# Kernel optimization log

Measured on AMD Instinct MI355X. Metric: run time of the kernel, lower is better.

## Reference

```python
import jax, jax.numpy as jnp
import numpy as np

N_SPOT, N_CITY, N_WORD = 20000, 2000, 20000
E_HAS, E_IN, E_DESC, E_RDESC = 100000, 100000, 400000, 400000
HID = 256


def setup_inputs() -> dict:
    key = jax.random.key(0)
    ks = jax.random.split(key, 48)

    def g(i, shape, s):
        return jax.random.normal(ks[i], shape, dtype=jnp.float32) * s

    inp = {}
    inp['x_spot'] = g(0, (N_SPOT, 2560), 0.5)
    inp['x_city'] = g(1, (N_CITY, 128), 0.5)
    inp['x_word'] = g(2, (N_WORD, 300), 0.5)
    inp['W_att'] = g(3, (4, 512, 128), 0.05)  # 4 heads, per_dim=128
    inp['q_att'] = g(4, (4, 128), 0.1)
    i = 5
    for n, d in [('w1_has_s', 128), ('w1_has_t', 512), ('w1_in_s', 512), ('w1_in_t', 128),
                 ('w1_desc_s', 300), ('w1_desc_t', 512), ('w1_rdesc_s', 512), ('w1_rdesc_t', 300)]:
        inp[n] = g(i, (d, HID), 0.05); i += 1
    for n in ['w2_has_s', 'w2_has_t', 'w2_in_s', 'w2_in_t', 'w2_desc_s', 'w2_desc_t', 'w2_rdesc_s', 'w2_rdesc_t']:
        inp[n] = g(i, (HID, HID), 0.05); i += 1
    for n in ['wl_spot', 'wl_city', 'wl_word']:
        inp[n] = g(i, (HID, 1), 0.05); i += 1
    for n in ['bl_spot', 'bl_city', 'bl_word']:
        inp[n] = jnp.zeros((1,), jnp.float32)
    for n, e, hi in [('e_has_src', E_HAS, N_CITY), ('e_has_tgt', E_HAS, N_SPOT),
                     ('e_in_src', E_IN, N_SPOT), ('e_in_tgt', E_IN, N_CITY),
                     ('e_desc_src', E_DESC, N_WORD), ('e_desc_tgt', E_DESC, N_SPOT),
                     ('e_rdesc_src', E_RDESC, N_SPOT), ('e_rdesc_tgt', E_RDESC, N_WORD)]:
        inp[n] = jax.random.randint(ks[i], (e,), 0, hi, dtype=jnp.int32); i += 1
    return inp


def _attention(x, W_att, q_att):
    # AttentionModule(input_dim=512, num_heads=4, split=5): (N, 2560) -> (N, 512)
    x = x.reshape(-1, 5, 512)
    xw = jnp.einsum('nsi,hio->hnso', x, W_att)                      # (4,N,5,128)
    a = jax.nn.leaky_relu(jnp.einsum('hnso,ho->hns', xw, q_att), 0.2)
    a = jax.nn.softmax(a, axis=2)                                   # softmax over split dim
    out = jnp.einsum('hnso,hns->hno', xw, a)                        # (4,N,128)
    return jnp.transpose(out, (1, 0, 2)).reshape(x.shape[0], 4 * 128)


def _scatter_mean(src, idx, n):
    s = jax.ops.segment_sum(src, idx, num_segments=n)
    c = jax.ops.segment_sum(jnp.ones((src.shape[0], 1), src.dtype), idx, num_segments=n)
    return s / jnp.maximum(c, 1.0)


def _edge(x_s, x_t, w_s, w_t, src, tgt):
    # per-edge-type linear, gather on source index, scatter-mean into targets
    msg = (x_s @ w_s)[src]
    return x_t @ w_t + _scatter_mean(msg, tgt, x_t.shape[0])


def _conv(xs, xc, xw, w, e):
    spot = _edge(xc, xs, w['has_s'], w['has_t'], e['has_src'], e['has_tgt']) \
         + _edge(xw, xs, w['desc_s'], w['desc_t'], e['desc_src'], e['desc_tgt'])
    city = _edge(xs, xc, w['in_s'], w['in_t'], e['in_src'], e['in_tgt'])
    word = _edge(xs, xw, w['rdesc_s'], w['rdesc_t'], e['rdesc_src'], e['rdesc_tgt'])
    # div[spot]=2, div[city]=div[word]=1; ReLU flag applies a second (idempotent) relu
    return jax.nn.relu(spot * 0.5), jax.nn.relu(city), jax.nn.relu(word)


def reference(x_spot, x_city, x_word, W_att, q_att,
              w1_has_s, w1_has_t, w1_in_s, w1_in_t, w1_desc_s, w1_desc_t, w1_rdesc_s, w1_rdesc_t,
              w2_has_s, w2_has_t, w2_in_s, w2_in_t, w2_desc_s, w2_desc_t, w2_rdesc_s, w2_rdesc_t,
              wl_spot, bl_spot, wl_city, bl_city, wl_word, bl_word,
              e_has_src, e_has_tgt, e_in_src, e_in_tgt, e_desc_src, e_desc_tgt, e_rdesc_src, e_rdesc_tgt):
    e = dict(has_src=e_has_src, has_tgt=e_has_tgt, in_src=e_in_src, in_tgt=e_in_tgt,
             desc_src=e_desc_src, desc_tgt=e_desc_tgt, rdesc_src=e_rdesc_src, rdesc_tgt=e_rdesc_tgt)
    w1 = dict(has_s=w1_has_s, has_t=w1_has_t, in_s=w1_in_s, in_t=w1_in_t,
              desc_s=w1_desc_s, desc_t=w1_desc_t, rdesc_s=w1_rdesc_s, rdesc_t=w1_rdesc_t)
    w2 = dict(has_s=w2_has_s, has_t=w2_has_t, in_s=w2_in_s, in_t=w2_in_t,
              desc_s=w2_desc_s, desc_t=w2_desc_t, rdesc_s=w2_rdesc_s, rdesc_t=w2_rdesc_t)
    xs = _attention(x_spot, W_att, q_att)  # multi=True path
    s1, c1, wd1 = _conv(xs, x_city, x_word, w1, e)
    s2, c2, wd2 = _conv(s1, c1, wd1, w2, e)
    out_spot = s2 @ wl_spot + bl_spot
    out_city = c2 @ wl_city + bl_city
    out_word = wd2 @ wl_word + bl_word
    # concat=True: mean over the two layer outputs per node type
    return ((s1 + s2) * 0.5, (c1 + c2) * 0.5, (wd1 + wd2) * 0.5, out_spot, out_city, out_word)
```

## Files before the change

### kernel.cpp

```cpp
#include <hip/hip_runtime.h>
#include <hip/hip_bf16.h>

#define HID 256
#define NSPOT 20000
#define NCITY 2000
#define NWORD 20000

typedef __attribute__((ext_vector_type(8))) short bhalf8;
typedef __attribute__((ext_vector_type(4))) float floatx4;

__global__ void wq_kernel(const float* __restrict__ W, const float* __restrict__ q,
                          float* __restrict__ wq) {
    int idx = blockIdx.x * 256 + threadIdx.x;
    if (idx >= 2048) return;
    int h = idx >> 9, i = idx & 511;
    const float* Wr = W + ((size_t)h * 512 + i) * 128;
    const float* qr = q + h * 128;
    float s = 0.f;
    #pragma unroll 4
    for (int o = 0; o < 128; o++) s += Wr[o] * qr[o];
    wq[idx] = s;
}

__global__ __launch_bounds__(256) void attn_kernel(const float* __restrict__ x,
                                                   const float* __restrict__ wq,
                                                   __hip_bfloat16* __restrict__ xbar) {
    __shared__ float xl[2560];
    __shared__ float al[4][8];
    int n = blockIdx.x;
    int tid = threadIdx.x;
    int wave = tid >> 6, lane = tid & 63;
    const float4* xr4 = (const float4*)(x + (size_t)n * 2560);
    for (int i = tid; i < 640; i += 256) ((float4*)xl)[i] = xr4[i];
    __syncthreads();
    const float* wqh = wq + wave * 512;
    for (int s = 0; s < 5; s++) {
        float a = 0.f;
        #pragma unroll
        for (int j = 0; j < 8; j++)
            a += xl[s * 512 + lane + j * 64] * wqh[lane + j * 64];
        #pragma unroll
        for (int off = 32; off > 0; off >>= 1) a += __shfl_down(a, off, 64);
        if (lane == 0) al[wave][s] = a;
    }
    __syncthreads();
    if (tid < 4) {
        float z[5]; float m = -1e30f;
        #pragma unroll
        for (int s = 0; s < 5; s++) {
            float v = al[tid][s];
            v = (v >= 0.f) ? v : 0.2f * v;
            z[s] = v; m = fmaxf(m, v);
        }
        float e[5]; float sum = 0.f;
        #pragma unroll
        for (int s = 0; s < 5; s++) { e[s] = __expf(z[s] - m); sum += e[s]; }
        float r = 1.f / sum;
        #pragma unroll
        for (int s = 0; s < 5; s++) al[tid][s] = e[s] * r;
    }
    __syncthreads();
    float a0 = al[wave][0], a1 = al[wave][1], a2 = al[wave][2], a3 = al[wave][3], a4 = al[wave][4];
    __hip_bfloat16* xo = xbar + ((size_t)wave * NSPOT + n) * 512;
    #pragma unroll
    for (int j = 0; j < 8; j++) {
        int i = lane + j * 64;
        float v = a0 * xl[i] + a1 * xl[512 + i] + a2 * xl[1024 + i] + a3 * xl[1536 + i] + a4 * xl[2048 + i];
        xo[i] = __float2bfloat16(v);
    }
}

#define KP 40
__global__ __launch_bounds__(256) void gemm_bf16(
    const __hip_bfloat16* __restrict__ A, int lda, long sA,
    const __hip_bfloat16* __restrict__ Bt, int ldb, long sB,
    float* __restrict__ C, int ldc,
    __hip_bfloat16* __restrict__ Cb, int ldcb, long sCb,
    int M, int N, int K) {
    __shared__ short As[128 * KP];
    __shared__ short Bs[128 * KP];
    int z = blockIdx.z;
    A += (size_t)z * sA;
    Bt += (size_t)z * sB;
    if (Cb) Cb += (size_t)z * sCb;
    int tid = threadIdx.x;
    int wave = tid >> 6, lane = tid & 63;
    int wr = wave & 1, wc = wave >> 1;
    int quad = lane >> 4, l16 = lane & 15;
    int rowbase = blockIdx.x * 128;
    int colbase = blockIdx.y * 128;
    int srow = tid >> 2;
    int skoff = (tid & 3) * 8;
    floatx4 acc[4][4];
    #pragma unroll
    for (int i = 0; i < 4; i++)
        #pragma unroll
        for (int j = 0; j < 4; j++)
            acc[i][j] = (floatx4){0.f, 0.f, 0.f, 0.f};

    for (int k0 = 0; k0 < K; k0 += 32) {
        #pragma unroll
        for (int i = 0; i < 2; i++) {
            int r = srow + i * 64;
            int gr = rowbase + r;
            int4 va = make_int4(0, 0, 0, 0);
            if (gr < M) va = *(const int4*)(A + (size_t)gr * lda + k0 + skoff);
            *(int4*)(As + r * KP + skoff) = va;
            int4 vb = *(const int4*)(Bt + (size_t)(colbase + r) * ldb + k0 + skoff);
            *(int4*)(Bs + r * KP + skoff) = vb;
        }
        __syncthreads();
        bhalf8 af[4], bfr[4];
        #pragma unroll
        for (int rt = 0; rt < 4; rt++)
            af[rt] = *(const bhalf8*)(As + (wr * 64 + rt * 16 + l16) * KP + quad * 8);
        #pragma unroll
        for (int ct = 0; ct < 4; ct++)
            bfr[ct] = *(const bhalf8*)(Bs + (wc * 64 + ct * 16 + l16) * KP + quad * 8);
        #pragma unroll
        for (int rt = 0; rt < 4; rt++)
            #pragma unroll
            for (int ct = 0; ct < 4; ct++)
                acc[rt][ct] = __builtin_amdgcn_mfma_f32_16x16x32_bf16(af[rt], bfr[ct], acc[rt][ct], 0, 0, 0);
        __syncthreads();
    }
    #pragma unroll
    for (int rt = 0; rt < 4; rt++) {
        #pragma unroll
        for (int r = 0; r < 4; r++) {
            int grow = rowbase + wr * 64 + rt * 16 + quad * 4 + r;
            if (grow < M) {
                #pragma unroll
                for (int ct = 0; ct < 4; ct++) {
                    int gcol = colbase + wc * 64 + ct * 16 + l16;
                    float v = acc[rt][ct][r];
                    if (C)  C[(size_t)grow * ldc + gcol] = v;
                    if (Cb) Cb[(size_t)grow * ldcb + gcol] = __float2bfloat16(v);
                }
            }
        }
    }
}

struct GemmDesc {
    const __hip_bfloat16* A;
    const __hip_bfloat16* Bt;
    float* C;
    __hip_bfloat16* Cb;
    int lda, ldb, ldc, ldcb, M, K;
};
struct GemmDesc8 { GemmDesc d[8]; };

__global__ __launch_bounds__(256) void gemm_bf16_grouped(GemmDesc8 descs) {
    GemmDesc g = descs.d[blockIdx.z];
    int rowbase = blockIdx.x * 128;
    if (rowbase >= g.M) return;
    __shared__ short As[128 * KP];
    __shared__ short Bs[128 * KP];
    int tid = threadIdx.x;
    int wave = tid >> 6, lane = tid & 63;
    int wr = wave & 1, wc = wave >> 1;
    int quad = lane >> 4, l16 = lane & 15;
    int colbase = blockIdx.y * 128;
    int srow = tid >> 2;
    int skoff = (tid & 3) * 8;
    floatx4 acc[4][4];
    #pragma unroll
    for (int i = 0; i < 4; i++)
        #pragma unroll
        for (int j = 0; j < 4; j++)
            acc[i][j] = (floatx4){0.f, 0.f, 0.f, 0.f};

    for (int k0 = 0; k0 < g.K; k0 += 32) {
        #pragma unroll
        for (int i = 0; i < 2; i++) {
            int r = srow + i * 64;
            int gr = rowbase + r;
            int4 va = make_int4(0, 0, 0, 0);
            if (gr < g.M) va = *(const int4*)(g.A + (size_t)gr * g.lda + k0 + skoff);
            *(int4*)(As + r * KP + skoff) = va;
            int4 vb = *(const int4*)(g.Bt + (size_t)(colbase + r) * g.ldb + k0 + skoff);
            *(int4*)(Bs + r * KP + skoff) = vb;
        }
        __syncthreads();
        bhalf8 af[4], bfr[4];
        #pragma unroll
        for (int rt = 0; rt < 4; rt++)
            af[rt] = *(const bhalf8*)(As + (wr * 64 + rt * 16 + l16) * KP + quad * 8);
        #pragma unroll
        for (int ct = 0; ct < 4; ct++)
            bfr[ct] = *(const bhalf8*)(Bs + (wc * 64 + ct * 16 + l16) * KP + quad * 8);
        #pragma unroll
        for (int rt = 0; rt < 4; rt++)
            #pragma unroll
            for (int ct = 0; ct < 4; ct++)
                acc[rt][ct] = __builtin_amdgcn_mfma_f32_16x16x32_bf16(af[rt], bfr[ct], acc[rt][ct], 0, 0, 0);
        __syncthreads();
    }
    #pragma unroll
    for (int rt = 0; rt < 4; rt++) {
        #pragma unroll
        for (int r = 0; r < 4; r++) {
            int grow = rowbase + wr * 64 + rt * 16 + quad * 4 + r;
            if (grow < g.M) {
                #pragma unroll
                for (int ct = 0; ct < 4; ct++) {
                    int gcol = colbase + wc * 64 + ct * 16 + l16;
                    float v = acc[rt][ct][r];
                    if (g.C)  g.C[(size_t)grow * g.ldc + gcol] = v;
                    if (g.Cb) g.Cb[(size_t)grow * g.ldcb + gcol] = __float2bfloat16(v);
                }
            }
        }
    }
}

struct TDesc { const float* in; __hip_bfloat16* out; int K; int N; int Kp; };
struct TDesc8 { TDesc d[8]; };
__global__ void transpose_cast_kernel(TDesc8 descs) {
    TDesc dsc = descs.d[blockIdx.z];
    __shared__ float tile[32][33];
    int k0 = blockIdx.x * 32, n0 = blockIdx.y * 32;
    if (k0 >= dsc.Kp || n0 >= dsc.N) return;
    int tn = threadIdx.x & 31, t8 = threadIdx.x >> 5;
    #pragma unroll
    for (int i = 0; i < 4; i++) {
        int k = k0 + t8 * 4 + i;
        float v = 0.f;
        if (k < dsc.K && n0 + tn < dsc.N) v = dsc.in[(size_t)k * dsc.N + n0 + tn];
        tile[t8 * 4 + i][tn] = v;
    }
    __syncthreads();
    int kk = threadIdx.x & 31, n8 = threadIdx.x >> 5;
    #pragma unroll
    for (int i = 0; i < 4; i++) {
        int n = n0 + n8 * 4 + i;
        int k = k0 + kk;
        if (n < dsc.N && k < dsc.Kp)
            dsc.out[(size_t)n * dsc.Kp + k] = __float2bfloat16(tile[kk][n8 * 4 + i]);
    }
}

__global__ void cast_kernel(const float* __restrict__ in, __hip_bfloat16* __restrict__ out, int n) {
    int i = blockIdx.x * 256 + threadIdx.x;
    if (i < n) out[i] = __float2bfloat16(in[i]);
}

__global__ void cast_pad_kernel(const float* __restrict__ in, __hip_bfloat16* __restrict__ out,
                                int rows, int K, int Kp) {
    int idx = blockIdx.x * 256 + threadIdx.x;
    if (idx >= rows * Kp) return;
    int r = idx / Kp, k = idx - r * Kp;
    out[idx] = (k < K) ? __float2bfloat16(in[(size_t)r * K + k]) : __float2bfloat16(0.f);
}

struct EdgeDesc { const int* src; const int* tgt; int E; int n;
                  int* deg; int* rp; int* cur; int* cs; };
struct EdgeDesc4 { EdgeDesc d[4]; };

__global__ void hist4_kernel(EdgeDesc4 ds) {
    EdgeDesc d = ds.d[blockIdx.y];
    int e = blockIdx.x * 256 + threadIdx.x;
    if (e < d.E) atomicAdd(&d.deg[d.tgt[e]], 1);
}

__global__ void scan4_kernel(EdgeDesc4 ds) {
    EdgeDesc dd = ds.d[blockIdx.x];
    __shared__ int partx[257];
    __shared__ int part[256];
    int tid = threadIdx.x;
    int n = dd.n;
    int chunk = (n + 255) / 256;
    int lo = tid * chunk;
    int hi = lo + chunk; if (hi > n) hi = n;
    int s = 0;
    for (int i = lo; i < hi; i++) s += dd.deg[i];
    part[tid] = s;
    __syncthreads();
    if (tid == 0) {
        int acc = 0;
        for (int i = 0; i < 256; i++) { partx[i] = acc; acc += part[i]; }
        partx[256] = acc;
    }
    __syncthreads();
    int acc = partx[tid];
    for (int i = lo; i < hi; i++) { dd.rp[i] = acc; dd.cur[i] = acc; acc += dd.deg[i]; }
    if (tid == 0) dd.rp[n] = partx[256];
}

__global__ void fill4_kernel(EdgeDesc4 ds) {
    EdgeDesc d = ds.d[blockIdx.y];
    int e = blockIdx.x * 256 + threadIdx.x;
    if (e >= d.E) return;
    int t = d.tgt[e];
    int pos = atomicAdd(&d.cur[t], 1);
    d.cs[pos] = d.src[e];
}

struct AggDesc { const __hip_bfloat16* msg; const int* rp; const int* cs; float* outm; };
struct AggDesc4 { AggDesc d[4]; int start1, start2, start3; };

__global__ __launch_bounds__(256) void agg4_kernel(AggDesc4 ds) {
    int bid = blockIdx.x;
    int gi = (bid >= ds.start1) + (bid >= ds.start2) + (bid >= ds.start3);
    int base = (gi == 0) ? 0 : (gi == 1) ? ds.start1 : (gi == 2) ? ds.start2 : ds.start3;
    AggDesc g = ds.d[gi];
    int t = bid - base;
    int d = threadIdx.x;
    int lo = g.rp[t], hi = g.rp[t + 1];
    float acc = 0.f;
    int i = lo;
    for (; i + 4 <= hi; i += 4) {
        int s0 = g.cs[i], s1 = g.cs[i + 1], s2 = g.cs[i + 2], s3 = g.cs[i + 3];
        float m0 = __bfloat162float(g.msg[(size_t)s0 * HID + d]);
        float m1 = __bfloat162float(g.msg[(size_t)s1 * HID + d]);
        float m2 = __bfloat162float(g.msg[(size_t)s2 * HID + d]);
        float m3 = __bfloat162float(g.msg[(size_t)s3 * HID + d]);
        acc += m0 + m1 + m2 + m3;
    }
    for (; i < hi; i++) acc += __bfloat162float(g.msg[(size_t)g.cs[i] * HID + d]);
    g.outm[(size_t)t * HID + d] = acc / fmaxf((float)(hi - lo), 1.f);
}

__global__ void combine_all(const float* Sa, const float* Sb, const float* mH, const float* mD,
                            float* so, __hip_bfloat16* sob,
                            const float* Sc, const float* mI, float* co, __hip_bfloat16* cob,
                            const float* Sw, const float* mR, float* wo, __hip_bfloat16* wob) {
    int bid = blockIdx.x;
    int tid = threadIdx.x;
    if (bid < NSPOT) {
        int idx = bid * 256 + tid;
        float v = fmaxf((Sa[idx] + Sb[idx] + mH[idx] + mD[idx]) * 0.5f, 0.f);
        so[idx] = v;
        if (sob) sob[idx] = __float2bfloat16(v);
    } else if (bid < NSPOT + NCITY) {
        int idx = (bid - NSPOT) * 256 + tid;
        float v = fmaxf(Sc[idx] + mI[idx], 0.f);
        co[idx] = v;
        if (cob) cob[idx] = __float2bfloat16(v);
    } else {
        int idx = (bid - NSPOT - NCITY) * 256 + tid;
        float v = fmaxf(Sw[idx] + mR[idx], 0.f);
        wo[idx] = v;
        if (wob) wob[idx] = __float2bfloat16(v);
    }
}

__global__ void mean3_kernel(const float* a0, const float* b0, float* o0, int n0,
                             const float* a1, const float* b1, float* o1, int n1,
                             const float* a2, const float* b2, float* o2, int n2) {
    int i = blockIdx.x * 256 + threadIdx.x;
    const float* a; const float* b; float* o;
    if (i < n0) { a = a0; b = b0; o = o0; }
    else if (i < n0 + n1) { a = a1; b = b1; o = o1; i -= n0; }
    else if (i < n0 + n1 + n2) { a = a2; b = b2; o = o2; i -= n0 + n1; }
    else return;
    float4 x = reinterpret_cast<const float4*>(a)[i];
    float4 y = reinterpret_cast<const float4*>(b)[i];
    reinterpret_cast<float4*>(o)[i] =
        make_float4((x.x + y.x) * 0.5f, (x.y + y.y) * 0.5f, (x.z + y.z) * 0.5f, (x.w + y.w) * 0.5f);
}

__global__ void rowdot3_kernel(const float* X0, const float* w0, const float* b0, float* o0, int B0,
                               const float* X1, const float* w1, const float* b1, float* o1, int B1,
                               const float* X2, const float* w2, const float* b2, float* o2, int B2) {
    int bid = blockIdx.x;
    const float* X; const float* w; const float* b; float* o; int M;
    if (bid < B0) { X = X0; w = w0; b = b0; o = o0; M = B0 * 4; }
    else if (bid < B0 + B1) { X = X1; w = w1; b = b1; o = o1; M = B1 * 4; bid -= B0; }
    else { X = X2; w = w2; b = b2; o = o2; M = B2 * 4; bid -= B0 + B1; }
    int row = bid * 4 + (threadIdx.x >> 6);
    if (row >= M) return;
    int lane = threadIdx.x & 63;
    const float* x = X + (size_t)row * HID;
    float s = 0.f;
    #pragma unroll
    for (int j = 0; j < 4; j++) s += x[lane + j * 64] * w[lane + j * 64];
    #pragma unroll
    for (int off = 32; off > 0; off >>= 1) s += __shfl_down(s, off, 64);
    if (lane == 0) o[row] = s + b[0];
}

extern "C" void kernel_launch(void* const* d_in, const int* in_sizes, int n_in,
                              void* d_out, int out_size, void* d_ws, size_t ws_size,
                              hipStream_t stream) {
    const float* x_spot   = (const float*)d_in[0];
    const float* x_city   = (const float*)d_in[1];
    const float* x_word   = (const float*)d_in[2];
    const float* W_att    = (const float*)d_in[3];
    const float* q_att    = (const float*)d_in[4];
    const float* w1[8] = { (const float*)d_in[5], (const float*)d_in[6], (const float*)d_in[7],
                           (const float*)d_in[8], (const float*)d_in[9], (const float*)d_in[10],
                           (const float*)d_in[11], (const float*)d_in[12] };
    const float* w2[8] = { (const float*)d_in[13], (const float*)d_in[14], (const float*)d_in[15],
                           (const float*)d_in[16], (const float*)d_in[17], (const float*)d_in[18],
                           (const float*)d_in[19], (const float*)d_in[20] };
    const float* wl_spot = (const float*)d_in[21];
    const float* wl_city = (const float*)d_in[22];
    const float* wl_word = (const float*)d_in[23];
    const float* bl_spot = (const float*)d_in[24];
    const float* bl_city = (const float*)d_in[25];
    const float* bl_word = (const float*)d_in[26];
    const int* e_has_src   = (const int*)d_in[27];
    const int* e_has_tgt   = (const int*)d_in[28];
    const int* e_in_src    = (const int*)d_in[29];
    const int* e_in_tgt    = (const int*)d_in[30];
    const int* e_desc_src  = (const int*)d_in[31];
    const int* e_desc_tgt  = (const int*)d_in[32];
    const int* e_rdesc_src = (const int*)d_in[33];
    const int* e_rdesc_tgt = (const int*)d_in[34];
    const int E_has   = in_sizes[27];
    const int E_in    = in_sizes[29];
    const int E_desc  = in_sizes[31];
    const int E_rdesc = in_sizes[33];

    float* out = (float*)d_out;
    float* wsf = (float*)d_ws;
    typedef __hip_bfloat16 bf;

    size_t o = 0;
    auto alloc = [&](size_t nfloats) { float* p = wsf + o; o += (nfloats + 15) & ~(size_t)15; return p; };
    float* wqb       = alloc(2048);
    bf* xs_bf        = (bf*)alloc((size_t)NSPOT * 512 / 2);
    bf* x_city_bf    = (bf*)alloc((size_t)NCITY * 128 / 2);
    bf* x_word_bf    = (bf*)alloc((size_t)NWORD * 320 / 2);
    bf* Wt_att       = (bf*)alloc((size_t)4 * 128 * 512 / 2);
    int K1[8]  = {128, 512, 512, 128, 300, 512, 512, 300};
    int Kp1[8] = {128, 512, 512, 128, 320, 512, 512, 320};
    bf* Wt1[8];
    for (int i = 0; i < 8; i++) Wt1[i] = (bf*)alloc((size_t)256 * Kp1[i] / 2);
    bf* Wt2[8];
    for (int i = 0; i < 8; i++) Wt2[i] = (bf*)alloc((size_t)256 * 256 / 2);
    float* Sa = alloc((size_t)NSPOT * HID);
    float* Sb = alloc((size_t)NSPOT * HID);
    float* Sc = alloc((size_t)NCITY * HID);
    float* Sw = alloc((size_t)NWORD * HID);
    float* m_has   = alloc((size_t)NSPOT * HID);
    float* m_desc  = alloc((size_t)NSPOT * HID);
    float* m_in    = alloc((size_t)NCITY * HID);
    float* m_rdesc = alloc((size_t)NWORD * HID);
    float* s1  = alloc((size_t)NSPOT * HID);
    float* c1  = alloc((size_t)NCITY * HID);
    float* wd1 = alloc((size_t)NWORD * HID);
    size_t regX = o;
    bf* xbar_bf = (bf*)(wsf + regX);
    size_t ox = regX;
    auto allocX = [&](size_t nfloats) { float* p = wsf + ox; ox += (nfloats + 15) & ~(size_t)15; return p; };
    bf* P_has_bf   = (bf*)allocX((size_t)NCITY * HID / 2);
    bf* P_in_bf    = (bf*)allocX((size_t)NSPOT * HID / 2);
    bf* P_desc_bf  = (bf*)allocX((size_t)NWORD * HID / 2);
    bf* P_rdesc_bf = (bf*)allocX((size_t)NSPOT * HID / 2);
    bf* s1b = (bf*)allocX((size_t)NSPOT * HID / 2);
    bf* c1b = (bf*)allocX((size_t)NCITY * HID / 2);
    bf* wd1b = (bf*)allocX((size_t)NWORD * HID / 2);
    o = regX + (size_t)4 * NSPOT * 512 / 2;
    float* s2  = m_has;
    float* c2  = m_in;
    float* wd2 = m_rdesc;
    int* wsi = (int*)(wsf + o);
    size_t io = 0;
    int* deg_has    = wsi + io; io += NSPOT;
    int* deg_desc   = wsi + io; io += NSPOT;
    int* deg_in     = wsi + io; io += NCITY;
    int* deg_rdesc  = wsi + io; io += NWORD;
    size_t deg_bytes = io * sizeof(int);
    int* rp_has     = wsi + io; io += NSPOT + 1;
    int* rp_desc    = wsi + io; io += NSPOT + 1;
    int* rp_in      = wsi + io; io += NCITY + 1;
    int* rp_rdesc   = wsi + io; io += NWORD + 1;
    int* cur_has    = wsi + io; io += NSPOT + 1;
    int* cur_desc   = wsi + io; io += NSPOT + 1;
    int* cur_in     = wsi + io; io += NCITY + 1;
    int* cur_rdesc  = wsi + io; io += NWORD + 1;
    int* cs_has     = wsi + io; io += E_has;
    int* cs_desc    = wsi + io; io += E_desc;
    int* cs_in      = wsi + io; io += E_in;
    int* cs_rdesc   = wsi + io; io += E_rdesc;
    (void)ws_size; (void)n_in; (void)out_size;

    {
        TDesc8 t{};
        for (int i = 0; i < 4; i++)
            t.d[i] = TDesc{ W_att + (size_t)i * 512 * 128, Wt_att + (size_t)i * 128 * 512, 512, 128, 512 };
        hipLaunchKernelGGL(transpose_cast_kernel, dim3(16, 4, 4), dim3(256), 0, stream, t);
    }
    {
        TDesc8 t{};
        for (int i = 0; i < 8; i++) t.d[i] = TDesc{ w1[i], Wt1[i], K1[i], 256, Kp1[i] };
        hipLaunchKernelGGL(transpose_cast_kernel, dim3(16, 8, 8), dim3(256), 0, stream, t);
    }
    {
        TDesc8 t{};
        for (int i = 0; i < 8; i++) t.d[i] = TDesc{ w2[i], Wt2[i], 256, 256, 256 };
        hipLaunchKernelGGL(transpose_cast_kernel, dim3(8, 8, 8), dim3(256), 0, stream, t);
    }
    hipLaunchKernelGGL(cast_kernel, dim3((NCITY * 128 + 255) / 256), dim3(256), 0, stream,
                       x_city, x_city_bf, NCITY * 128);
    hipLaunchKernelGGL(cast_pad_kernel, dim3((NWORD * 320 + 255) / 256), dim3(256), 0, stream,
                       x_word, x_word_bf, NWORD, 300, 320);

    EdgeDesc4 ed;
    ed.d[0] = EdgeDesc{ e_has_src,   e_has_tgt,   E_has,   NSPOT, deg_has,   rp_has,   cur_has,   cs_has };
    ed.d[1] = EdgeDesc{ e_desc_src,  e_desc_tgt,  E_desc,  NSPOT, deg_desc,  rp_desc,  cur_desc,  cs_desc };
    ed.d[2] = EdgeDesc{ e_in_src,    e_in_tgt,    E_in,    NCITY, deg_in,    rp_in,    cur_in,    cs_in };
    ed.d[3] = EdgeDesc{ e_rdesc_src, e_rdesc_tgt, E_rdesc, NWORD, deg_rdesc, rp_rdesc, cur_rdesc, cs_rdesc };
    int Emax = E_has;
    if (E_desc > Emax) Emax = E_desc;
    if (E_in > Emax) Emax = E_in;
    if (E_rdesc > Emax) Emax = E_rdesc;
    hipMemsetAsync((void*)deg_has, 0, deg_bytes, stream);
    hipLaunchKernelGGL(hist4_kernel, dim3((Emax + 255) / 256, 4), dim3(256), 0, stream, ed);
    hipLaunchKernelGGL(scan4_kernel, dim3(4), dim3(256), 0, stream, ed);
    hipLaunchKernelGGL(fill4_kernel, dim3((Emax + 255) / 256, 4), dim3(256), 0, stream, ed);

    hipLaunchKernelGGL(wq_kernel, dim3(8), dim3(256), 0, stream, W_att, q_att, wqb);
    hipLaunchKernelGGL(attn_kernel, dim3(NSPOT), dim3(256), 0, stream, x_spot, wqb, xbar_bf);
    {
        dim3 g((NSPOT + 127) / 128, 1, 4);
        hipLaunchKernelGGL(gemm_bf16, g, dim3(256), 0, stream,
                           xbar_bf, 512, (long)NSPOT * 512, Wt_att, 512, (long)128 * 512,
                           nullptr, 0, xs_bf, 512, 128, NSPOT, 128, 512);
    }

    int gx = (NSPOT + 127) / 128;

    {
        GemmDesc8 gd;
        gd.d[0] = GemmDesc{ x_city_bf, Wt1[0], nullptr, P_has_bf,   128, 128, 0, HID, NCITY, 128 };
        gd.d[1] = GemmDesc{ xs_bf,     Wt1[1], Sa,      nullptr,    512, 512, HID, 0, NSPOT, 512 };
        gd.d[2] = GemmDesc{ xs_bf,     Wt1[2], nullptr, P_in_bf,    512, 512, 0, HID, NSPOT, 512 };
        gd.d[3] = GemmDesc{ x_city_bf, Wt1[3], Sc,      nullptr,    128, 128, HID, 0, NCITY, 128 };
        gd.d[4] = GemmDesc{ x_word_bf, Wt1[4], nullptr, P_desc_bf,  320, 320, 0, HID, NWORD, 320 };
        gd.d[5] = GemmDesc{ xs_bf,     Wt1[5], Sb,      nullptr,    512, 512, HID, 0, NSPOT, 512 };
        gd.d[6] = GemmDesc{ xs_bf,     Wt1[6], nullptr, P_rdesc_bf, 512, 512, 0, HID, NSPOT, 512 };
        gd.d[7] = GemmDesc{ x_word_bf, Wt1[7], Sw,      nullptr,    320, 320, HID, 0, NWORD, 320 };
        hipLaunchKernelGGL(gemm_bf16_grouped, dim3(gx, 2, 8), dim3(256), 0, stream, gd);
    }

    AggDesc4 ag;
    ag.start1 = NSPOT; ag.start2 = 2 * NSPOT; ag.start3 = 2 * NSPOT + NCITY;
    int agg_blocks = 2 * NSPOT + NCITY + NWORD;
    ag.d[0] = AggDesc{ P_has_bf,   rp_has,   cs_has,   m_has };
    ag.d[1] = AggDesc{ P_desc_bf,  rp_desc,  cs_desc,  m_desc };
    ag.d[2] = AggDesc{ P_in_bf,    rp_in,    cs_in,    m_in };
    ag.d[3] = AggDesc{ P_rdesc_bf, rp_rdesc, cs_rdesc, m_rdesc };
    hipLaunchKernelGGL(agg4_kernel, dim3(agg_blocks), dim3(256), 0, stream, ag);
    hipLaunchKernelGGL(combine_all, dim3(NSPOT + NCITY + NWORD), dim3(256), 0, stream,
                       Sa, Sb, m_has, m_desc, s1, s1b,
                       Sc, m_in, c1, c1b,
                       Sw, m_rdesc, wd1, wd1b);

    {
        GemmDesc8 gd;
        gd.d[0] = GemmDesc{ c1b,  Wt2[0], nullptr, P_has_bf,   HID, HID, 0, HID, NCITY, HID };
        gd.d[1] = GemmDesc{ s1b,  Wt2[1], Sa,      nullptr,    HID, HID, HID, 0, NSPOT, HID };
        gd.d[2] = GemmDesc{ s1b,  Wt2[2], nullptr, P_in_bf,    HID, HID, 0, HID, NSPOT, HID };
        gd.d[3] = GemmDesc{ c1b,  Wt2[3], Sc,      nullptr,    HID, HID, HID, 0, NCITY, HID };
        gd.d[4] = GemmDesc{ wd1b, Wt2[4], nullptr, P_desc_bf,  HID, HID, 0, HID, NWORD, HID };
        gd.d[5] = GemmDesc{ s1b,  Wt2[5], Sb,      nullptr,    HID, HID, HID, 0, NSPOT, HID };
        gd.d[6] = GemmDesc{ s1b,  Wt2[6], nullptr, P_rdesc_bf, HID, HID, 0, HID, NSPOT, HID };
        gd.d[7] = GemmDesc{ wd1b, Wt2[7], Sw,      nullptr,    HID, HID, HID, 0, NWORD, HID };
        hipLaunchKernelGGL(gemm_bf16_grouped, dim3(gx, 2, 8), dim3(256), 0, stream, gd);
    }

    hipLaunchKernelGGL(agg4_kernel, dim3(agg_blocks), dim3(256), 0, stream, ag);
    hipLaunchKernelGGL(combine_all, dim3(NSPOT + NCITY + NWORD), dim3(256), 0, stream,
                       Sa, Sb, m_has, m_desc, s2, (bf*)nullptr,
                       Sc, m_in, c2, (bf*)nullptr,
                       Sw, m_rdesc, wd2, (bf*)nullptr);

    float* out0 = out;
    float* out1 = out + (size_t)NSPOT * HID;
    float* out2 = out1 + (size_t)NCITY * HID;
    float* out3 = out2 + (size_t)NWORD * HID;
    float* out4 = out3 + NSPOT;
    float* out5 = out4 + NCITY;
    int n4s = NSPOT * HID / 4, n4c = NCITY * HID / 4, n4w = NWORD * HID / 4;
    int n4tot = n4s + n4c + n4w;
    hipLaunchKernelGGL(mean3_kernel, dim3((n4tot + 255) / 256), dim3(256), 0, stream,
                       s1, s2, out0, n4s, c1, c2, out1, n4c, wd1, wd2, out2, n4w);
    hipLaunchKernelGGL(rowdot3_kernel, dim3(NSPOT / 4 + NCITY / 4 + NWORD / 4), dim3(256), 0, stream,
                       s2, wl_spot, bl_spot, out3, NSPOT / 4,
                       c2, wl_city, bl_city, out4, NCITY / 4,
                       wd2, wl_word, bl_word, out5, NWORD / 4);
}
```

Measured before the change: 1.013 ms.

## Vectorize aggregation per wavefront and fuse layer-2 combine, mean and readout

The aggregation kernel now assigns one 64-lane wavefront per destination row, with each lane loading four bf16 values at once, so one 256-thread block handles four rows instead of one. The layer-1 combine is vectorized with float4 and always writes the bf16 copy. The second-layer combine, the layer-mean output and the final row-dot readout are merged into a single finale kernel, so s2/c2/wd2 are never written to memory and then reread. This is meant to cut memory traffic and launch count, in exchange for more branching per row in the fused kernels.

```diff
diff --git a/kernel.cpp b/kernel.cpp
--- a/kernel.cpp
+++ b/kernel.cpp
@@ -8,6 +8,17 @@
 
 typedef __attribute__((ext_vector_type(8))) short bhalf8;
 typedef __attribute__((ext_vector_type(4))) float floatx4;
+
+__device__ inline float bf2f(unsigned short u) {
+    union { unsigned int i; float f; } v; v.i = (unsigned int)u << 16; return v.f;
+}
+__device__ inline unsigned short f2bf(float f) {
+    __hip_bfloat16 b = __float2bfloat16(f);
+    return *reinterpret_cast<unsigned short*>(&b);
+}
+__device__ inline float4 ld4(const float* p, size_t off) {
+    return *reinterpret_cast<const float4*>(p + off);
+}
 
 __global__ void wq_kernel(const float* __restrict__ W, const float* __restrict__ q,
                           float* __restrict__ wq) {
@@ -300,85 +311,114 @@
 struct AggDesc { const __hip_bfloat16* msg; const int* rp; const int* cs; float* outm; };
 struct AggDesc4 { AggDesc d[4]; int start1, start2, start3; };
 
-__global__ __launch_bounds__(256) void agg4_kernel(AggDesc4 ds) {
-    int bid = blockIdx.x;
-    int gi = (bid >= ds.start1) + (bid >= ds.start2) + (bid >= ds.start3);
+__global__ __launch_bounds__(256) void agg4_kernel(AggDesc4 ds, int nrows) {
+    int row = blockIdx.x * 4 + (threadIdx.x >> 6);
+    if (row >= nrows) return;
+    int lane = threadIdx.x & 63;
+    int gi = (row >= ds.start1) + (row >= ds.start2) + (row >= ds.start3);
     int base = (gi == 0) ? 0 : (gi == 1) ? ds.start1 : (gi == 2) ? ds.start2 : ds.start3;
     AggDesc g = ds.d[gi];
-    int t = bid - base;
-    int d = threadIdx.x;
+    int t = row - base;
     int lo = g.rp[t], hi = g.rp[t + 1];
-    float acc = 0.f;
+    float a0 = 0.f, a1 = 0.f, a2 = 0.f, a3 = 0.f;
+    int doff = lane * 4;
     int i = lo;
     for (; i + 4 <= hi; i += 4) {
         int s0 = g.cs[i], s1 = g.cs[i + 1], s2 = g.cs[i + 2], s3 = g.cs[i + 3];
-        float m0 = __bfloat162float(g.msg[(size_t)s0 * HID + d]);
-        float m1 = __bfloat162float(g.msg[(size_t)s1 * HID + d]);
-        float m2 = __bfloat162float(g.msg[(size_t)s2 * HID + d]);
-        float m3 = __bfloat162float(g.msg[(size_t)s3 * HID + d]);
-        acc += m0 + m1 + m2 + m3;
-    }
-    for (; i < hi; i++) acc += __bfloat162float(g.msg[(size_t)g.cs[i] * HID + d]);
-    g.outm[(size_t)t * HID + d] = acc / fmaxf((float)(hi - lo), 1.f);
-}
-
-__global__ void combine_all(const float* Sa, const float* Sb, const float* mH, const float* mD,
-                            float* so, __hip_bfloat16* sob,
-                            const float* Sc, const float* mI, float* co, __hip_bfloat16* cob,
-                            const float* Sw, const float* mR, float* wo, __hip_bfloat16* wob) {
-    int bid = blockIdx.x;
-    int tid = threadIdx.x;
-    if (bid < NSPOT) {
-        int idx = bid * 256 + tid;
-        float v = fmaxf((Sa[idx] + Sb[idx] + mH[idx] + mD[idx]) * 0.5f, 0.f);
-        so[idx] = v;
-        if (sob) sob[idx] = __float2bfloat16(v);
-    } else if (bid < NSPOT + NCITY) {
-        int idx = (bid - NSPOT) * 256 + tid;
-        float v = fmaxf(Sc[idx] + mI[idx], 0.f);
-        co[idx] = v;
-        if (cob) cob[idx] = __float2bfloat16(v);
+        ushort4 u0 = *(const ushort4*)(g.msg + (size_t)s0 * HID + doff);
+        ushort4 u1 = *(const ushort4*)(g.msg + (size_t)s1 * HID + doff);
+        ushort4 u2 = *(const ushort4*)(g.msg + (size_t)s2 * HID + doff);
+        ushort4 u3 = *(const ushort4*)(g.msg + (size_t)s3 * HID + doff);
+        a0 += (bf2f(u0.x) + bf2f(u1.x)) + (bf2f(u2.x) + bf2f(u3.x));
+        a1 += (bf2f(u0.y) + bf2f(u1.y)) + (bf2f(u2.y) + bf2f(u3.y));
+        a2 += (bf2f(u0.z) + bf2f(u1.z)) + (bf2f(u2.z) + bf2f(u3.z));
+        a3 += (bf2f(u0.w) + bf2f(u1.w)) + (bf2f(u2.w) + bf2f(u3.w));
+    }
+    for (; i < hi; i++) {
+        ushort4 u = *(const ushort4*)(g.msg + (size_t)g.cs[i] * HID + doff);
+        a0 += bf2f(u.x); a1 += bf2f(u.y); a2 += bf2f(u.z); a3 += bf2f(u.w);
+    }
+    float inv = 1.f / fmaxf((float)(hi - lo), 1.f);
+    float4 o = make_float4(a0 * inv, a1 * inv, a2 * inv, a3 * inv);
+    *reinterpret_cast<float4*>(g.outm + (size_t)t * HID + doff) = o;
+}
+
+__global__ __launch_bounds__(256) void combine1v_kernel(
+    const float* Sa, const float* Sb, const float* mH, const float* mD,
+    float* s1, __hip_bfloat16* s1b,
+    const float* Sc, const float* mI, float* c1, __hip_bfloat16* c1b,
+    const float* Sw, const float* mR, float* wd1, __hip_bfloat16* wd1b) {
+    int row = blockIdx.x * 4 + (threadIdx.x >> 6);
+    if (row >= NSPOT + NCITY + NWORD) return;
+    int lane = threadIdx.x & 63;
+    float4 v; float* of; __hip_bfloat16* ob; size_t off;
+    if (row < NSPOT) {
+        off = (size_t)row * HID + lane * 4;
+        float4 a = ld4(Sa, off), b = ld4(Sb, off), h = ld4(mH, off), d = ld4(mD, off);
+        v = make_float4(fmaxf((a.x + b.x + h.x + d.x) * 0.5f, 0.f),
+                        fmaxf((a.y + b.y + h.y + d.y) * 0.5f, 0.f),
+                        fmaxf((a.z + b.z + h.z + d.z) * 0.5f, 0.f),
+                        fmaxf((a.w + b.w + h.w + d.w) * 0.5f, 0.f));
+        of = s1; ob = s1b;
+    } else if (row < NSPOT + NCITY) {
+        off = (size_t)(row - NSPOT) * HID + lane * 4;
+        float4 a = ld4(Sc, off), m = ld4(mI, off);
+        v = make_float4(fmaxf(a.x + m.x, 0.f), fmaxf(a.y + m.y, 0.f),
+                        fmaxf(a.z + m.z, 0.f), fmaxf(a.w + m.w, 0.f));
+        of = c1; ob = c1b;
     } else {
-        int idx = (bid - NSPOT - NCITY) * 256 + tid;
-        float v = fmaxf(Sw[idx] + mR[idx], 0.f);
-        wo[idx] = v;
-        if (wob) wob[idx] = __float2bfloat16(v);
-    }
-}
-
-__global__ void mean3_kernel(const float* a0, const float* b0, float* o0, int n0,
-                             const float* a1, const float* b1, float* o1, int n1,
-                             const float* a2, const float* b2, float* o2, int n2) {
-    int i = blockIdx.x * 256 + threadIdx.x;
-    const float* a; const float* b; float* o;
-    if (i < n0) { a = a0; b = b0; o = o0; }
-    else if (i < n0 + n1) { a = a1; b = b1; o = o1; i -= n0; }
-    else if (i < n0 + n1 + n2) { a = a2; b = b2; o = o2; i -= n0 + n1; }
-    else return;
-    float4 x = reinterpret_cast<const float4*>(a)[i];
-    float4 y = reinterpret_cast<const float4*>(b)[i];
-    reinterpret_cast<float4*>(o)[i] =
-        make_float4((x.x + y.x) * 0.5f, (x.y + y.y) * 0.5f, (x.z + y.z) * 0.5f, (x.w + y.w) * 0.5f);
-}
-
-__global__ void rowdot3_kernel(const float* X0, const float* w0, const float* b0, float* o0, int B0,
-                               const float* X1, const float* w1, const float* b1, float* o1, int B1,
-                               const float* X2, const float* w2, const float* b2, float* o2, int B2) {
-    int bid = blockIdx.x;
-    const float* X; const float* w; const float* b; float* o; int M;
-    if (bid < B0) { X = X0; w = w0; b = b0; o = o0; M = B0 * 4; }
-    else if (bid < B0 + B1) { X = X1; w = w1; b = b1; o = o1; M = B1 * 4; bid -= B0; }
-    else { X = X2; w = w2; b = b2; o = o2; M = B2 * 4; bid -= B0 + B1; }
-    int row = bid * 4 + (threadIdx.x >> 6);
-    if (row >= M) return;
+        off = (size_t)(row - NSPOT - NCITY) * HID + lane * 4;
+        float4 a = ld4(Sw, off), m = ld4(mR, off);
+        v = make_float4(fmaxf(a.x + m.x, 0.f), fmaxf(a.y + m.y, 0.f),
+                        fmaxf(a.z + m.z, 0.f), fmaxf(a.w + m.w, 0.f));
+        of = wd1; ob = wd1b;
+    }
+    *reinterpret_cast<float4*>(of + off) = v;
+    ushort4 ub = make_ushort4(f2bf(v.x), f2bf(v.y), f2bf(v.z), f2bf(v.w));
+    *reinterpret_cast<ushort4*>((unsigned short*)ob + off) = ub;
+}
+
+__global__ __launch_bounds__(256) void finale_kernel(
+    const float* Sa, const float* Sb, const float* mH, const float* mD,
+    const float* s1, float* out0, const float* wls, const float* bls, float* out3,
+    const float* Sc, const float* mI, const float* c1, float* out1,
+    const float* wlc, const float* blc, float* out4,
+    const float* Sw, const float* mR, const float* wd1, float* out2,
+    const float* wlw, const float* blw, float* out5) {
+    int row = blockIdx.x * 4 + (threadIdx.x >> 6);
+    if (row >= NSPOT + NCITY + NWORD) return;
     int lane = threadIdx.x & 63;
-    const float* x = X + (size_t)row * HID;
-    float s = 0.f;
-    #pragma unroll
-    for (int j = 0; j < 4; j++) s += x[lane + j * 64] * w[lane + j * 64];
-    #pragma unroll
-    for (int off = 32; off > 0; off >>= 1) s += __shfl_down(s, off, 64);
-    if (lane == 0) o[row] = s + b[0];
+    float4 v, p; const float* wl; const float* bl; float* om; float* od;
+    int r; size_t off;
+    if (row < NSPOT) {
+        r = row; off = (size_t)r * HID + lane * 4;
+        float4 a = ld4(Sa, off), b = ld4(Sb, off), h = ld4(mH, off), d = ld4(mD, off);
+        v = make_float4(fmaxf((a.x + b.x + h.x + d.x) * 0.5f, 0.f),
+                        fmaxf((a.y + b.y + h.y + d.y) * 0.5f, 0.f),
+                        fmaxf((a.z + b.z + h.z + d.z) * 0.5f, 0.f),
+                        fmaxf((a.w + b.w + h.w + d.w) * 0.5f, 0.f));
+        p = ld4(s1, off); wl = wls; bl = bls; om = out0; od = out3;
+    } else if (row < NSPOT + NCITY) {
+        r = row - NSPOT; off = (size_t)r * HID + lane * 4;
+        float4 a = ld4(Sc, off), m = ld4(mI, off);
+        v = make_float4(fmaxf(a.x + m.x, 0.f), fmaxf(a.y + m.y, 0.f),
+                        fmaxf(a.z + m.z, 0.f), fmaxf(a.w + m.w, 0.f));
+        p = ld4(c1, off); wl = wlc; bl = blc; om = out1; od = out4;
+    } else {
+        r = row - NSPOT - NCITY; off = (size_t)r * HID + lane * 4;
+        float4 a = ld4(Sw, off), m = ld4(mR, off);
+        v = make_float4(fmaxf(a.x + m.x, 0.f), fmaxf(a.y + m.y, 0.f),
+                        fmaxf(a.z + m.z, 0.f), fmaxf(a.w + m.w, 0.f));
+        p = ld4(wd1, off); wl = wlw; bl = blw; om = out2; od = out5;
+    }
+    float4 m4 = make_float4((p.x + v.x) * 0.5f, (p.y + v.y) * 0.5f,
+                            (p.z + v.z) * 0.5f, (p.w + v.w) * 0.5f);
+    *reinterpret_cast<float4*>(om + off) = m4;
+    float4 w = *reinterpret_cast<const float4*>(wl + lane * 4);
+    float s = v.x * w.x + v.y * w.y + v.z * w.z + v.w * w.w;
+    #pragma unroll
+    for (int o2 = 32; o2 > 0; o2 >>= 1) s += __shfl_down(s, o2, 64);
+    if (lane == 0) od[r] = s + bl[0];
 }
 
 extern "C" void kernel_launch(void* const* d_in, const int* in_sizes, int n_in,
@@ -454,9 +494,6 @@
     bf* c1b = (bf*)allocX((size_t)NCITY * HID / 2);
     bf* wd1b = (bf*)allocX((size_t)NWORD * HID / 2);
     o = regX + (size_t)4 * NSPOT * 512 / 2;
-    float* s2  = m_has;
-    float* c2  = m_in;
-    float* wd2 = m_rdesc;
     int* wsi = (int*)(wsf + o);
     size_t io = 0;
     int* deg_has    = wsi + io; io += NSPOT;
@@ -539,13 +576,13 @@
 
     AggDesc4 ag;
     ag.start1 = NSPOT; ag.start2 = 2 * NSPOT; ag.start3 = 2 * NSPOT + NCITY;
-    int agg_blocks = 2 * NSPOT + NCITY + NWORD;
+    int agg_rows = 2 * NSPOT + NCITY + NWORD;
     ag.d[0] = AggDesc{ P_has_bf,   rp_has,   cs_has,   m_has };
     ag.d[1] = AggDesc{ P_desc_bf,  rp_desc,  cs_desc,  m_desc };
     ag.d[2] = AggDesc{ P_in_bf,    rp_in,    cs_in,    m_in };
     ag.d[3] = AggDesc{ P_rdesc_bf, rp_rdesc, cs_rdesc, m_rdesc };
-    hipLaunchKernelGGL(agg4_kernel, dim3(agg_blocks), dim3(256), 0, stream, ag);
-    hipLaunchKernelGGL(combine_all, dim3(NSPOT + NCITY + NWORD), dim3(256), 0, stream,
+    hipLaunchKernelGGL(agg4_kernel, dim3((agg_rows + 3) / 4), dim3(256), 0, stream, ag, agg_rows);
+    hipLaunchKernelGGL(combine1v_kernel, dim3((NSPOT + NCITY + NWORD) / 4), dim3(256), 0, stream,
                        Sa, Sb, m_has, m_desc, s1, s1b,
                        Sc, m_in, c1, c1b,
                        Sw, m_rdesc, wd1, wd1b);
@@ -563,11 +600,7 @@
         hipLaunchKernelGGL(gemm_bf16_grouped, dim3(gx, 2, 8), dim3(256), 0, stream, gd);
     }
 
-    hipLaunchKernelGGL(agg4_kernel, dim3(agg_blocks), dim3(256), 0, stream, ag);
-    hipLaunchKernelGGL(combine_all, dim3(NSPOT + NCITY + NWORD), dim3(256), 0, stream,
-                       Sa, Sb, m_has, m_desc, s2, (bf*)nullptr,
-                       Sc, m_in, c2, (bf*)nullptr,
-                       Sw, m_rdesc, wd2, (bf*)nullptr);
+    hipLaunchKernelGGL(agg4_kernel, dim3((agg_rows + 3) / 4), dim3(256), 0, stream, ag, agg_rows);
 
     float* out0 = out;
     float* out1 = out + (size_t)NSPOT * HID;
@@ -575,12 +608,8 @@
     float* out3 = out2 + (size_t)NWORD * HID;
     float* out4 = out3 + NSPOT;
     float* out5 = out4 + NCITY;
-    int n4s = NSPOT * HID / 4, n4c = NCITY * HID / 4, n4w = NWORD * HID / 4;
-    int n4tot = n4s + n4c + n4w;
-    hipLaunchKernelGGL(mean3_kernel, dim3((n4tot + 255) / 256), dim3(256), 0, stream,
-                       s1, s2, out0, n4s, c1, c2, out1, n4c, wd1, wd2, out2, n4w);
-    hipLaunchKernelGGL(rowdot3_kernel, dim3(NSPOT / 4 + NCITY / 4 + NWORD / 4), dim3(256), 0, stream,
-                       s2, wl_spot, bl_spot, out3, NSPOT / 4,
-                       c2, wl_city, bl_city, out4, NCITY / 4,
-                       wd2, wl_word, bl_word, out5, NWORD / 4);
-}
+    hipLaunchKernelGGL(finale_kernel, dim3((NSPOT + NCITY + NWORD) / 4), dim3(256), 0, stream,
+                       Sa, Sb, m_has, m_desc, s1, out0, wl_spot, bl_spot, out3,
+                       Sc, m_in, c1, out1, wl_city, bl_city, out4,
+                       Sw, m_rdesc, wd1, out2, wl_word, bl_word, out5);
+}
```

Measured after the change: 960.8 us. 5.2% less time.
